# Kernel tuning notes

Hardware: AMD Instinct MI355X
Metric: run time of the kernel (lower is better)

Reference implementation:

```python
import jax, jax.numpy as jnp
import numpy as np

B, T, I, H, L = 256, 512, 64, 256, 2


def _lstm_layer(x, Wih, Whh, bih, bhh):
    # x: [B, T, Din]; Wih: [4H, Din]; Whh: [4H, H]; gate order i,f,g,o (PyTorch)
    Hdim = Whh.shape[1]
    # Precompute input projections for all timesteps (one big GEMM)
    x_proj = jnp.einsum('btd,gd->btg', x, Wih) + bih + bhh  # [B, T, 4H]
    x_proj = jnp.transpose(x_proj, (1, 0, 2))  # [T, B, 4H]

    def step(carry, xt):
        h, c = carry
        gates = xt + h @ Whh.T  # [B, 4H]
        i, f, g, o = jnp.split(gates, 4, axis=-1)
        i = jax.nn.sigmoid(i)
        f = jax.nn.sigmoid(f)
        g = jnp.tanh(g)
        o = jax.nn.sigmoid(o)
        c = f * c + i * g
        h = o * jnp.tanh(c)
        return (h, c), h

    b = x.shape[0]
    h0 = jnp.zeros((b, Hdim), dtype=x.dtype)
    c0 = jnp.zeros((b, Hdim), dtype=x.dtype)
    _, hs = jax.lax.scan(step, (h0, c0), x_proj)  # hs: [T, B, H]
    return jnp.transpose(hs, (1, 0, 2))  # [B, T, H]


def setup_inputs() -> dict:
    key = jax.random.key(0)
    ks = jax.random.split(key, 12)
    s_in = 1.0 / np.sqrt(H)
    inp = {
        'x': jax.random.normal(ks[0], (B, T, I), dtype=jnp.float32),
        'Wih0': jax.random.uniform(ks[1], (4 * H, I), minval=-s_in, maxval=s_in),
        'Whh0': jax.random.uniform(ks[2], (4 * H, H), minval=-s_in, maxval=s_in),
        'bih0': jax.random.uniform(ks[3], (4 * H,), minval=-s_in, maxval=s_in),
        'bhh0': jax.random.uniform(ks[4], (4 * H,), minval=-s_in, maxval=s_in),
        'Wih1': jax.random.uniform(ks[5], (4 * H, H), minval=-s_in, maxval=s_in),
        'Whh1': jax.random.uniform(ks[6], (4 * H, H), minval=-s_in, maxval=s_in),
        'bih1': jax.random.uniform(ks[7], (4 * H,), minval=-s_in, maxval=s_in),
        'bhh1': jax.random.uniform(ks[8], (4 * H,), minval=-s_in, maxval=s_in),
        'Wfc': jax.random.uniform(ks[9], (1, H), minval=-s_in, maxval=s_in),
        'bfc': jax.random.uniform(ks[10], (1,), minval=-s_in, maxval=s_in),
    }
    return inp


def reference(x, Wih0, Whh0, bih0, bhh0, Wih1, Whh1, bih1, bhh1, Wfc, bfc):
    h1 = _lstm_layer(x, Wih0, Whh0, bih0, bhh0)   # [B, T, H]
    h2 = _lstm_layer(h1, Wih1, Whh1, bih1, bhh1)  # [B, T, H]
    last = h2[:, -1, :]                           # [B, H]
    return last @ Wfc.T + bfc                     # [B, 1]
```

## Files before the change

kernel.cpp:

```cpp
#include <hip/hip_runtime.h>

#define TT   512
#define IDIM 64
#define HDIM 256

typedef short  short8  __attribute__((ext_vector_type(8)));
typedef short  short4v __attribute__((ext_vector_type(4)));
typedef float  f32x4   __attribute__((ext_vector_type(4)));
typedef unsigned long long u64;

__device__ __forceinline__ short f2bf(float f) {
    unsigned u = __float_as_uint(f);
    u = u + 0x7FFFu + ((u >> 16) & 1u);
    return (short)(u >> 16);
}
__device__ __forceinline__ float bf2f(short h) {
    return __uint_as_float(((unsigned)(unsigned short)h) << 16);
}
__device__ __forceinline__ float sigm(float x)  { return 1.0f / (1.0f + __expf(-x)); }
__device__ __forceinline__ float tanh_(float x) { return 2.0f / (1.0f + __expf(-2.0f * x)) - 1.0f; }

__global__ __launch_bounds__(256, 1) void lstm_fused(
    const float* __restrict__ x,
    const float* __restrict__ Wih0, const float* __restrict__ Whh0,
    const float* __restrict__ bih0, const float* __restrict__ bhh0,
    const float* __restrict__ Wih1, const float* __restrict__ Whh1,
    const float* __restrict__ bih1, const float* __restrict__ bhh1,
    const float* __restrict__ Wfc,  const float* __restrict__ bfc,
    float* __restrict__ out, char* __restrict__ ws)
{
    int*   flags = (int*)ws;
    short* h0buf = (short*)(ws + 1024);
    short* h1buf = h0buf + 2 * 16 * 16 * 256;

    const int blk   = blockIdx.x;
    const int grp   = ((blk & 7) << 1) | ((blk >> 3) & 1);
    const int chunk = blk >> 4;
    const int tid   = threadIdx.x;
    const int lane  = tid & 63;
    const int wave  = tid >> 6;
    const int quad  = lane >> 4;
    const int nn    = lane & 15;

    __shared__ short A0[16][328];
    __shared__ short A1[16][520];
    __shared__ float gbuf[2][4][16][16];
    __shared__ float red[16][16];
    __shared__ __align__(16) short hls[2][16][16];
    __shared__ float ldspad[5120];

    for (int i = tid; i < 16 * 328; i += 256) (&A0[0][0])[i] = 0;
    for (int i = tid; i < 16 * 520; i += 256) (&A1[0][0])[i] = 0;

    const int wrow = wave * HDIM + chunk * 16 + nn;
    short8 w0f[10];
    short8 w1f[16];
#pragma unroll
    for (int kb = 0; kb < 10; ++kb)
#pragma unroll
        for (int j = 0; j < 8; ++j) {
            int k = kb * 32 + quad * 8 + j;
            float v = (k < 64) ? Wih0[wrow * IDIM + k] : Whh0[wrow * HDIM + (k - 64)];
            w0f[kb][j] = f2bf(v);
        }
#pragma unroll
    for (int kb = 0; kb < 16; ++kb)
#pragma unroll
        for (int j = 0; j < 8; ++j) {
            int k = kb * 32 + quad * 8 + j;
            float v = (k < 256) ? Wih1[wrow * HDIM + k] : Whh1[wrow * HDIM + (k - 256)];
            w1f[kb][j] = f2bf(v);
        }
    const float bias0 = bih0[wrow] + bhh0[wrow];
    const float bias1 = bih1[wrow] + bhh1[wrow];

    const int em = tid >> 4;
    const int ej = tid & 15;
    float c0 = 0.0f, c1 = 0.0f;

    auto load_x = [&](int t) {
        const float4 v = *(const float4*)&x[((size_t)(grp * 16 + em) * TT + t) * IDIM + ej * 4];
        short4v sv;
        sv[0] = f2bf(v.x); sv[1] = f2bf(v.y); sv[2] = f2bf(v.z); sv[3] = f2bf(v.w);
        *(short4v*)&A0[em][ej * 4] = sv;
    };

    __syncthreads();
    load_x(0);
    __syncthreads();

    for (int s = 0; s <= TT; ++s) {
        const int par = s & 1;

        if (s < TT) {
            f32x4 acc = {0.f, 0.f, 0.f, 0.f};
#pragma unroll
            for (int kb = 0; kb < 10; ++kb) {
                short8 a = *(const short8*)&A0[nn][kb * 32 + quad * 8];
                acc = __builtin_amdgcn_mfma_f32_16x16x32_bf16(a, w0f[kb], acc, 0, 0, 0);
            }
#pragma unroll
            for (int r = 0; r < 4; ++r)
                gbuf[0][wave][quad * 4 + r][nn] = acc[r] + bias0;
        }
        if (s >= 1) {
            f32x4 acc = {0.f, 0.f, 0.f, 0.f};
#pragma unroll
            for (int kb = 0; kb < 16; ++kb) {
                short8 a = *(const short8*)&A1[nn][kb * 32 + quad * 8];
                acc = __builtin_amdgcn_mfma_f32_16x16x32_bf16(a, w1f[kb], acc, 0, 0, 0);
            }
#pragma unroll
            for (int r = 0; r < 4; ++r)
                gbuf[1][wave][quad * 4 + r][nn] = acc[r] + bias1;
        }
        __syncthreads();

        if (s < TT) {
            float gi = sigm (gbuf[0][0][em][ej]);
            float gf = sigm (gbuf[0][1][em][ej]);
            float gg = tanh_(gbuf[0][2][em][ej]);
            float go = sigm (gbuf[0][3][em][ej]);
            c0 = gf * c0 + gi * gg;
            hls[0][em][ej] = f2bf(go * tanh_(c0));
        }
        if (s >= 1) {
            float gi = sigm (gbuf[1][0][em][ej]);
            float gf = sigm (gbuf[1][1][em][ej]);
            float gg = tanh_(gbuf[1][2][em][ej]);
            float go = sigm (gbuf[1][3][em][ej]);
            c1 = gf * c1 + gi * gg;
            hls[1][em][ej] = f2bf(go * tanh_(c1));
        } else {
            hls[1][em][ej] = 0;
        }
        __syncthreads();

        if (tid < 64) {
            const int wm = tid >> 2;
            const int wp = tid & 3;
            const u64 v0 = *(const u64*)&hls[0][wm][wp * 4];
            const u64 v1 = *(const u64*)&hls[1][wm][wp * 4];
            const size_t base = ((size_t)(par * 16 + grp) * 16 + wm) * 256 + chunk * 16 + wp * 4;
            __hip_atomic_store((u64*)&h0buf[base], v0, __ATOMIC_RELAXED, __HIP_MEMORY_SCOPE_AGENT);
            __hip_atomic_store((u64*)&h1buf[base], v1, __ATOMIC_RELAXED, __HIP_MEMORY_SCOPE_AGENT);
            asm volatile("s_waitcnt vmcnt(0)" ::: "memory");
            if (tid == 0)
                __hip_atomic_store(&flags[grp * 16 + chunk], s + 1,
                                   __ATOMIC_RELAXED, __HIP_MEMORY_SCOPE_AGENT);
        }

        if (s + 1 < TT) load_x(s + 1);

        if (tid < 16) {
            while (__hip_atomic_load(&flags[grp * 16 + tid],
                                     __ATOMIC_RELAXED, __HIP_MEMORY_SCOPE_AGENT) < s + 1) {}
        }
        __syncthreads();

        if (s < TT) {
            const size_t base = ((size_t)(par * 16 + grp) * 16 + em) * 256 + ej * 16;
            const u64* s0 = (const u64*)&h0buf[base];
            u64 v0 = __hip_atomic_load(&s0[0], __ATOMIC_RELAXED, __HIP_MEMORY_SCOPE_AGENT);
            u64 v1 = __hip_atomic_load(&s0[1], __ATOMIC_RELAXED, __HIP_MEMORY_SCOPE_AGENT);
            u64 v2 = __hip_atomic_load(&s0[2], __ATOMIC_RELAXED, __HIP_MEMORY_SCOPE_AGENT);
            u64 v3 = __hip_atomic_load(&s0[3], __ATOMIC_RELAXED, __HIP_MEMORY_SCOPE_AGENT);
            u64* d0 = (u64*)&A0[em][64 + ej * 16];
            u64* d1 = (u64*)&A1[em][ej * 16];
            d0[0] = v0; d0[1] = v1; d0[2] = v2; d0[3] = v3;
            d1[0] = v0; d1[1] = v1; d1[2] = v2; d1[3] = v3;
        }
        if (s >= 1) {
            const size_t base = ((size_t)(par * 16 + grp) * 16 + em) * 256 + ej * 16;
            const u64* s1 = (const u64*)&h1buf[base];
            u64 v0 = __hip_atomic_load(&s1[0], __ATOMIC_RELAXED, __HIP_MEMORY_SCOPE_AGENT);
            u64 v1 = __hip_atomic_load(&s1[1], __ATOMIC_RELAXED, __HIP_MEMORY_SCOPE_AGENT);
            u64 v2 = __hip_atomic_load(&s1[2], __ATOMIC_RELAXED, __HIP_MEMORY_SCOPE_AGENT);
            u64 v3 = __hip_atomic_load(&s1[3], __ATOMIC_RELAXED, __HIP_MEMORY_SCOPE_AGENT);
            u64* d2 = (u64*)&A1[em][256 + ej * 16];
            d2[0] = v0; d2[1] = v1; d2[2] = v2; d2[3] = v3;
        }
        __syncthreads();
    }

    {
        float part = 0.f;
#pragma unroll
        for (int kk = 0; kk < 16; ++kk) {
            int k = ej * 16 + kk;
            part += bf2f(A1[em][256 + k]) * Wfc[k];
        }
        red[em][ej] = part;
    }
    __syncthreads();
    if (chunk == 0 && tid < 16) {
        float sum = bfc[0];
#pragma unroll
        for (int c = 0; c < 16; ++c) sum += red[tid][c];
        out[grp * 16 + tid] = sum;
    }

    if (gridDim.x > 100000) { ldspad[tid] = bias0; out[0] = ldspad[255 - tid]; }
}

extern "C" void kernel_launch(void* const* d_in, const int* in_sizes, int n_in,
                              void* d_out, int out_size, void* d_ws, size_t ws_size,
                              hipStream_t stream) {
    (void)in_sizes; (void)n_in; (void)out_size; (void)ws_size;
    const float* x    = (const float*)d_in[0];
    const float* Wih0 = (const float*)d_in[1];
    const float* Whh0 = (const float*)d_in[2];
    const float* bih0 = (const float*)d_in[3];
    const float* bhh0 = (const float*)d_in[4];
    const float* Wih1 = (const float*)d_in[5];
    const float* Whh1 = (const float*)d_in[6];
    const float* bih1 = (const float*)d_in[7];
    const float* bhh1 = (const float*)d_in[8];
    const float* Wfc  = (const float*)d_in[9];
    const float* bfc  = (const float*)d_in[10];

    lstm_fused<<<256, 256, 0, stream>>>(x, Wih0, Whh0, bih0, bhh0,
                                        Wih1, Whh1, bih1, bhh1, Wfc, bfc,
                                        (float*)d_out, (char*)d_ws);
}
```

Baseline: 1.795 ms.

## Replace flag-based inter-block sync with poisoned data-word polling and split MFMA accumulators

Drops the per-block flag store and spin-wait plus the extra barrier. Instead, consumers poll the h-state words directly, using a 4-deep ring buffer with poison values and bitwise-inverted payloads so a ready word cannot be mistaken for poison or zero. This removes one global round trip and one __syncthreads per timestep. The MFMA chains are also split into two independent accumulators to shorten the dependency chain. The cost is more polling traffic and reliance on 64-bit stores being visible atomically.

After: 2.631 ms. +46.5%, slower.

```diff
diff --git a/kernel.cpp b/kernel.cpp
--- a/kernel.cpp
+++ b/kernel.cpp
@@ -9,6 +9,8 @@
 typedef float  f32x4   __attribute__((ext_vector_type(4)));
 typedef unsigned long long u64;
 
+#define POIS 0xAAAAAAAAAAAAAAAAull
+
 __device__ __forceinline__ short f2bf(float f) {
     unsigned u = __float_as_uint(f);
     u = u + 0x7FFFu + ((u >> 16) & 1u);
@@ -19,6 +21,8 @@
 }
 __device__ __forceinline__ float sigm(float x)  { return 1.0f / (1.0f + __expf(-x)); }
 __device__ __forceinline__ float tanh_(float x) { return 2.0f / (1.0f + __expf(-2.0f * x)) - 1.0f; }
+
+__device__ __forceinline__ bool rdy(u64 w) { return (w != POIS) & (w != 0ull); }
 
 __global__ __launch_bounds__(256, 1) void lstm_fused(
     const float* __restrict__ x,
@@ -29,9 +33,8 @@
     const float* __restrict__ Wfc,  const float* __restrict__ bfc,
     float* __restrict__ out, char* __restrict__ ws)
 {
-    int*   flags = (int*)ws;
-    short* h0buf = (short*)(ws + 1024);
-    short* h1buf = h0buf + 2 * 16 * 16 * 256;
+    short* h0buf = (short*)ws;
+    short* h1buf = h0buf + 4 * 16 * 16 * 256;
 
     const int blk   = blockIdx.x;
     const int grp   = ((blk & 7) << 1) | ((blk >> 3) & 1);
@@ -90,26 +93,38 @@
     __syncthreads();
 
     for (int s = 0; s <= TT; ++s) {
-        const int par = s & 1;
+        if (tid < 64) {
+            const int wm = tid >> 2, wp = tid & 3;
+            const size_t pb = (((size_t)(((s + 2) & 3) * 16 + grp)) * 16 + wm) * 256
+                              + chunk * 16 + wp * 4;
+            __hip_atomic_store((u64*)&h0buf[pb], POIS, __ATOMIC_RELAXED, __HIP_MEMORY_SCOPE_AGENT);
+            __hip_atomic_store((u64*)&h1buf[pb], POIS, __ATOMIC_RELAXED, __HIP_MEMORY_SCOPE_AGENT);
+        }
 
         if (s < TT) {
-            f32x4 acc = {0.f, 0.f, 0.f, 0.f};
-#pragma unroll
-            for (int kb = 0; kb < 10; ++kb) {
-                short8 a = *(const short8*)&A0[nn][kb * 32 + quad * 8];
-                acc = __builtin_amdgcn_mfma_f32_16x16x32_bf16(a, w0f[kb], acc, 0, 0, 0);
-            }
+            f32x4 accA = {0.f, 0.f, 0.f, 0.f}, accB = {0.f, 0.f, 0.f, 0.f};
+#pragma unroll
+            for (int kb = 0; kb < 10; kb += 2) {
+                short8 a0v = *(const short8*)&A0[nn][kb * 32 + quad * 8];
+                short8 a1v = *(const short8*)&A0[nn][(kb + 1) * 32 + quad * 8];
+                accA = __builtin_amdgcn_mfma_f32_16x16x32_bf16(a0v, w0f[kb],     accA, 0, 0, 0);
+                accB = __builtin_amdgcn_mfma_f32_16x16x32_bf16(a1v, w0f[kb + 1], accB, 0, 0, 0);
+            }
+            const f32x4 acc = accA + accB;
 #pragma unroll
             for (int r = 0; r < 4; ++r)
                 gbuf[0][wave][quad * 4 + r][nn] = acc[r] + bias0;
         }
         if (s >= 1) {
-            f32x4 acc = {0.f, 0.f, 0.f, 0.f};
-#pragma unroll
-            for (int kb = 0; kb < 16; ++kb) {
-                short8 a = *(const short8*)&A1[nn][kb * 32 + quad * 8];
-                acc = __builtin_amdgcn_mfma_f32_16x16x32_bf16(a, w1f[kb], acc, 0, 0, 0);
-            }
+            f32x4 accA = {0.f, 0.f, 0.f, 0.f}, accB = {0.f, 0.f, 0.f, 0.f};
+#pragma unroll
+            for (int kb = 0; kb < 16; kb += 2) {
+                short8 a0v = *(const short8*)&A1[nn][kb * 32 + quad * 8];
+                short8 a1v = *(const short8*)&A1[nn][(kb + 1) * 32 + quad * 8];
+                accA = __builtin_amdgcn_mfma_f32_16x16x32_bf16(a0v, w1f[kb],     accA, 0, 0, 0);
+                accB = __builtin_amdgcn_mfma_f32_16x16x32_bf16(a1v, w1f[kb + 1], accB, 0, 0, 0);
+            }
+            const f32x4 acc = accA + accB;
 #pragma unroll
             for (int r = 0; r < 4; ++r)
                 gbuf[1][wave][quad * 4 + r][nn] = acc[r] + bias1;
@@ -137,48 +152,67 @@
         __syncthreads();
 
         if (tid < 64) {
-            const int wm = tid >> 2;
-            const int wp = tid & 3;
-            const u64 v0 = *(const u64*)&hls[0][wm][wp * 4];
-            const u64 v1 = *(const u64*)&hls[1][wm][wp * 4];
-            const size_t base = ((size_t)(par * 16 + grp) * 16 + wm) * 256 + chunk * 16 + wp * 4;
-            __hip_atomic_store((u64*)&h0buf[base], v0, __ATOMIC_RELAXED, __HIP_MEMORY_SCOPE_AGENT);
-            __hip_atomic_store((u64*)&h1buf[base], v1, __ATOMIC_RELAXED, __HIP_MEMORY_SCOPE_AGENT);
+            const int wm = tid >> 2, wp = tid & 3;
+            const u64 v0 = ~(*(const u64*)&hls[0][wm][wp * 4]);
+            const u64 v1 = ~(*(const u64*)&hls[1][wm][wp * 4]);
+            const size_t db = (((size_t)((s & 3) * 16 + grp)) * 16 + wm) * 256
+                              + chunk * 16 + wp * 4;
             asm volatile("s_waitcnt vmcnt(0)" ::: "memory");
-            if (tid == 0)
-                __hip_atomic_store(&flags[grp * 16 + chunk], s + 1,
-                                   __ATOMIC_RELAXED, __HIP_MEMORY_SCOPE_AGENT);
+            __hip_atomic_store((u64*)&h0buf[db], v0, __ATOMIC_RELAXED, __HIP_MEMORY_SCOPE_AGENT);
+            __hip_atomic_store((u64*)&h1buf[db], v1, __ATOMIC_RELAXED, __HIP_MEMORY_SCOPE_AGENT);
         }
 
         if (s + 1 < TT) load_x(s + 1);
 
-        if (tid < 16) {
-            while (__hip_atomic_load(&flags[grp * 16 + tid],
-                                     __ATOMIC_RELAXED, __HIP_MEMORY_SCOPE_AGENT) < s + 1) {}
-        }
-        __syncthreads();
-
-        if (s < TT) {
-            const size_t base = ((size_t)(par * 16 + grp) * 16 + em) * 256 + ej * 16;
-            const u64* s0 = (const u64*)&h0buf[base];
-            u64 v0 = __hip_atomic_load(&s0[0], __ATOMIC_RELAXED, __HIP_MEMORY_SCOPE_AGENT);
-            u64 v1 = __hip_atomic_load(&s0[1], __ATOMIC_RELAXED, __HIP_MEMORY_SCOPE_AGENT);
-            u64 v2 = __hip_atomic_load(&s0[2], __ATOMIC_RELAXED, __HIP_MEMORY_SCOPE_AGENT);
-            u64 v3 = __hip_atomic_load(&s0[3], __ATOMIC_RELAXED, __HIP_MEMORY_SCOPE_AGENT);
-            u64* d0 = (u64*)&A0[em][64 + ej * 16];
-            u64* d1 = (u64*)&A1[em][ej * 16];
-            d0[0] = v0; d0[1] = v1; d0[2] = v2; d0[3] = v3;
-            d1[0] = v0; d1[1] = v1; d1[2] = v2; d1[3] = v3;
-        }
-        if (s >= 1) {
-            const size_t base = ((size_t)(par * 16 + grp) * 16 + em) * 256 + ej * 16;
-            const u64* s1 = (const u64*)&h1buf[base];
-            u64 v0 = __hip_atomic_load(&s1[0], __ATOMIC_RELAXED, __HIP_MEMORY_SCOPE_AGENT);
-            u64 v1 = __hip_atomic_load(&s1[1], __ATOMIC_RELAXED, __HIP_MEMORY_SCOPE_AGENT);
-            u64 v2 = __hip_atomic_load(&s1[2], __ATOMIC_RELAXED, __HIP_MEMORY_SCOPE_AGENT);
-            u64 v3 = __hip_atomic_load(&s1[3], __ATOMIC_RELAXED, __HIP_MEMORY_SCOPE_AGENT);
-            u64* d2 = (u64*)&A1[em][256 + ej * 16];
-            d2[0] = v0; d2[1] = v1; d2[2] = v2; d2[3] = v3;
+        {
+            const bool g0 = (s < TT), g1 = (s >= 1);
+            const size_t rb = (((size_t)((s & 3) * 16 + grp)) * 16 + em) * 256;
+            const u64* p0 = (const u64*)&h0buf[rb];
+            const u64* p1 = (const u64*)&h1buf[rb];
+            u64 w0[4] = {POIS, POIS, POIS, POIS};
+            u64 w1[4] = {POIS, POIS, POIS, POIS};
+            if (g0) {
+#pragma unroll
+                for (int i = 0; i < 4; ++i)
+                    w0[i] = __hip_atomic_load(p0 + ej + 16 * i,
+                                              __ATOMIC_RELAXED, __HIP_MEMORY_SCOPE_AGENT);
+            }
+            if (g1) {
+#pragma unroll
+                for (int i = 0; i < 4; ++i)
+                    w1[i] = __hip_atomic_load(p1 + ej + 16 * i,
+                                              __ATOMIC_RELAXED, __HIP_MEMORY_SCOPE_AGENT);
+            }
+            for (;;) {
+                bool done = true;
+#pragma unroll
+                for (int i = 0; i < 4; ++i) {
+                    if (g0 && !rdy(w0[i])) {
+                        done = false;
+                        w0[i] = __hip_atomic_load(p0 + ej + 16 * i,
+                                                  __ATOMIC_RELAXED, __HIP_MEMORY_SCOPE_AGENT);
+                    }
+                    if (g1 && !rdy(w1[i])) {
+                        done = false;
+                        w1[i] = __hip_atomic_load(p1 + ej + 16 * i,
+                                                  __ATOMIC_RELAXED, __HIP_MEMORY_SCOPE_AGENT);
+                    }
+                }
+                if (done) break;
+            }
+            if (g0) {
+#pragma unroll
+                for (int i = 0; i < 4; ++i) {
+                    const u64 d = ~w0[i];
+                    *(u64*)&A0[em][64 + (ej + 16 * i) * 4] = d;
+                    *(u64*)&A1[em][     (ej + 16 * i) * 4] = d;
+                }
+            }
+            if (g1) {
+#pragma unroll
+                for (int i = 0; i < 4; ++i)
+                    *(u64*)&A1[em][256 + (ej + 16 * i) * 4] = ~w1[i];
+            }
         }
         __syncthreads();
     }
```
